# Optimization experiments

Measured on AMD Instinct MI355X. Metric: run time of the kernel, lower is better.

## Reference

```python
import jax, jax.numpy as jnp
import numpy as np

B, C, H, W = 8, 256, 64, 64
K = 64  # tfam_channels

def _conv3x3(x, w, b):
    # x: [B,C,H,W], w: [O,I,3,3]
    y = jax.lax.conv_general_dilated(x, w, window_strides=(1, 1), padding='SAME',
                                     dimension_numbers=('NCHW', 'OIHW', 'NCHW'))
    return y + b[None, :, None, None]

def setup_inputs() -> dict:
    key = jax.random.key(0)
    ks = jax.random.split(key, 5)
    s1 = 1.0 / np.sqrt(C)
    s3 = 1.0 / np.sqrt(C * 9)
    return {
        'x': jax.random.normal(ks[0], (B, C, H, W), jnp.float32),
        'top_w': jax.random.normal(ks[1], (K, C), jnp.float32) * s1,
        'top_b': jnp.zeros((K,), jnp.float32),
        'center_w': jax.random.normal(ks[2], (K, C), jnp.float32) * s1,
        'center_b': jnp.zeros((K,), jnp.float32),
        'bottom_w': jax.random.normal(ks[3], (C, C, 3, 3), jnp.float32) * s3,
        'bottom_b': jnp.zeros((C,), jnp.float32),
        'out_w': jax.random.normal(ks[4], (C, C, 3, 3), jnp.float32) * s3,
        'out_b': jnp.zeros((C,), jnp.float32),
    }

def reference(x, top_w, top_b, center_w, center_b, bottom_w, bottom_b, out_w, out_b):
    b, c, h, w = x.shape
    hw = h * w
    # 1x1 convs as channel contractions
    x_top = jnp.einsum('bchw,kc->bkhw', x, top_w) + top_b[None, :, None, None]
    x_center = jnp.einsum('bchw,kc->bkhw', x, center_w) + center_b[None, :, None, None]
    x_bottom = _conv3x3(x, bottom_w, bottom_b)

    x_top = x_top.reshape(b, -1, hw)                     # [B,K,HW]
    x_center = x_center.reshape(b, -1, hw)               # [B,K,HW]
    x_bot = x_bottom.reshape(b, c, hw).transpose(0, 2, 1)  # [B,HW,C]

    sp_map = jnp.einsum('bkn,bkm->bnm', x_center, x_top)  # [B,HW,HW]
    # global softmax over the entire flattened map per batch element
    sp_map = jax.nn.softmax(sp_map.reshape(b, -1), axis=1).reshape(b, hw, hw)
    sp_map = jnp.einsum('bnm,bmc->bnc', sp_map, x_bot)    # [B,HW,C]
    # faithful raw reshape (as in the torch code: no transpose)
    sp_map = sp_map.reshape(b, c, h, w)
    y = x + sp_map
    return _conv3x3(y, out_w, out_b)
```

## Files before the change

### kernel.cpp

```cpp
#include <hip/hip_runtime.h>

using bf16x8 = __attribute__((ext_vector_type(8))) short;
using f16x8  = __attribute__((ext_vector_type(8))) _Float16;
using f32x4  = __attribute__((ext_vector_type(4))) float;

#define DEVI static __device__ __forceinline__

DEVI unsigned short f2bf(float f){
  unsigned u = __builtin_bit_cast(unsigned, f);
  u += 0x7fffu + ((u >> 16) & 1u);
  return (unsigned short)(u >> 16);
}
DEVI float bf2f(unsigned short h){
  unsigned u = ((unsigned)h) << 16;
  return __builtin_bit_cast(float, u);
}
DEVI unsigned short f2h(float f){
  _Float16 h = (_Float16)f;
  return __builtin_bit_cast(unsigned short, h);
}
DEVI f32x4 zf4(){ f32x4 z; z[0]=0.f; z[1]=0.f; z[2]=0.f; z[3]=0.f; return z; }

__global__ __launch_bounds__(256) void k_prep(
    const float* __restrict__ top_w, const float* __restrict__ cen_w,
    const float* __restrict__ bot_w, const float* __restrict__ out_w,
    float* __restrict__ wTt, float* __restrict__ wTc,
    unsigned short* __restrict__ apb, unsigned short* __restrict__ apo){
  int i = blockIdx.x * 256 + threadIdx.x;
  if (i < 64 * 256){
    int c = i >> 6, k = i & 63;
    wTt[i] = top_w[k * 256 + c];
    wTc[i] = cen_w[k * 256 + c];
  }
  if (i < 9 * 256 * 256){
    int tau = i >> 16, oc = i & 65535;
    apb[i] = f2bf(bot_w[oc * 9 + tau]);
    apo[i] = f2bf(out_w[oc * 9 + tau]);
  }
}

__global__ __launch_bounds__(256) void k_topcenter(
    const float* __restrict__ x,
    const float* __restrict__ wTt, const float* __restrict__ wTc,
    const float* __restrict__ top_b, const float* __restrict__ cen_b,
    unsigned short* __restrict__ tT16, unsigned short* __restrict__ cT16){
  __shared__ float xs[16][256];
  int bid = blockIdx.x;
  int b = bid & 7, z = (bid >> 3) & 1, nt = (bid >> 4) & 15, kq = bid >> 8;
  int t = threadIdx.x;
  int n = nt * 256 + t;
  int k0 = kq * 16;
  const float* wT   = z ? wTc : wTt;
  const float* bias = z ? cen_b : top_b;
  unsigned short* o16 = z ? cT16 : tT16;
  const float scale = z ? 1.0f : 1.4426950408889634f;
  const float* xb = x + ((size_t)b << 20);

  float acc[16];
  #pragma unroll
  for (int k = 0; k < 16; k++) acc[k] = 0.f;

  for (int cc = 0; cc < 256; cc += 16){
    __syncthreads();
    #pragma unroll
    for (int r = 0; r < 16; r++)
      xs[r][t] = xb[((size_t)(cc + r) << 12) + nt * 256 + t];
    __syncthreads();
    #pragma unroll
    for (int r = 0; r < 16; r++){
      float xv = xs[r][t];
      const float* wr = wT + (cc + r) * 64 + k0;
      #pragma unroll
      for (int k = 0; k < 16; k++) acc[k] = fmaf(wr[k], xv, acc[k]);
    }
  }
  size_t base = (((size_t)b << 12) + n) * 64 + k0;
  #pragma unroll
  for (int k8 = 0; k8 < 16; k8 += 8){
    bf16x8 v8;
    #pragma unroll
    for (int j = 0; j < 8; j++)
      v8[j] = (short)f2h((acc[k8 + j] + bias[k0 + k8 + j]) * scale);
    *(bf16x8*)(o16 + base + k8) = v8;
  }
}

__global__ __launch_bounds__(256) void k_transx(
    const float* __restrict__ x, unsigned short* __restrict__ ocl){
  __shared__ float tile[32][33];
  int b = blockIdx.z, ct = blockIdx.y, pt = blockIdx.x;
  int tx = threadIdx.x & 31, ty = threadIdx.x >> 5;
  size_t bo = (size_t)b << 20;
  int c0 = ct * 32, p0 = pt * 32;
  #pragma unroll
  for (int q = 0; q < 4; q++){
    int c = c0 + ty + q * 8;
    tile[ty + q * 8][tx] = x[bo + ((size_t)c << 12) + p0 + tx];
  }
  __syncthreads();
  #pragma unroll
  for (int q = 0; q < 4; q++){
    int p = p0 + ty + q * 8;
    ocl[bo + ((size_t)p << 8) + c0 + tx] = f2bf(tile[tx][ty + q * 8]);
  }
}

__global__ __launch_bounds__(256) void k_transy(
    const float* __restrict__ x, const unsigned short* __restrict__ U0,
    const unsigned short* __restrict__ U1, const float* __restrict__ Z,
    unsigned short* __restrict__ ocl){
  __shared__ float tile[32][33];
  int b = blockIdx.z, ct = blockIdx.y, pt = blockIdx.x;
  int tx = threadIdx.x & 31, ty = threadIdx.x >> 5;
  size_t bo = (size_t)b << 20;
  int c0 = ct * 32, p0 = pt * 32;
  float invZ = 1.0f / Z[b];
  #pragma unroll
  for (int q = 0; q < 4; q++){
    int c = c0 + ty + q * 8;
    size_t idx = bo + ((size_t)c << 12) + p0 + tx;
    float u = bf2f(U0[idx]);
    if (U1) u += bf2f(U1[idx]);
    tile[ty + q * 8][tx] = fmaf(u, invZ, x[idx]);
  }
  __syncthreads();
  #pragma unroll
  for (int q = 0; q < 4; q++){
    int p = p0 + ty + q * 8;
    ocl[bo + ((size_t)p << 8) + c0 + tx] = f2bf(tile[tx][ty + q * 8]);
  }
}

template<int OUTF32>
__global__ __launch_bounds__(256, 4) void k_conv3(
    const unsigned short* __restrict__ incl,
    const unsigned short* __restrict__ ap,
    const float* __restrict__ bias, void* __restrict__ outp){
  __shared__ unsigned short Xs[3][64][72];
  int bid = blockIdx.x;
  int b = bid & 7, h = (bid >> 3) & 63, oh = bid >> 9;
  int t = threadIdx.x, wv = t >> 6, l = t & 63, lr = l & 15, g = l >> 4;
  int o0 = oh * 128 + wv * 32;
  const unsigned short* inb = incl + ((size_t)b << 20);

  f32x4 acc[2][4];
  #pragma unroll
  for (int a = 0; a < 2; a++)
    #pragma unroll
    for (int c = 0; c < 4; c++) acc[a][c] = zf4();

  int sw = t >> 2, sco = (t & 3) * 16;
  const bf16x8 zero8 = {0,0,0,0,0,0,0,0};

  bf16x8 st[3][2];
  #pragma unroll
  for (int r = 0; r < 3; r++){
    int h2 = h + r - 1;
    bool v = (unsigned)h2 < 64u;
    #pragma unroll
    for (int u = 0; u < 2; u++)
      st[r][u] = v ? *(const bf16x8*)(inb + (((size_t)(h2 * 64 + sw)) << 8)
                                      + sco + u * 8)
                   : zero8;
  }

  for (int cc = 0; cc < 256; cc += 64){
    __syncthreads();
    #pragma unroll
    for (int r = 0; r < 3; r++)
      #pragma unroll
      for (int u = 0; u < 2; u++)
        *(bf16x8*)(&Xs[r][sw][sco + u * 8]) = st[r][u];
    __syncthreads();
    if (cc < 192){
      #pragma unroll
      for (int r = 0; r < 3; r++){
        int h2 = h + r - 1;
        bool v = (unsigned)h2 < 64u;
        #pragma unroll
        for (int u = 0; u < 2; u++)
          st[r][u] = v ? *(const bf16x8*)(inb + (((size_t)(h2 * 64 + sw)) << 8)
                                          + cc + 64 + sco + u * 8)
                       : zero8;
      }
    }
    #pragma unroll
    for (int tau = 0; tau < 9; tau++){
      int dy = tau / 3 - 1, dx = tau % 3 - 1;
      #pragma unroll
      for (int kf = 0; kf < 2; kf++){
        bf16x8 af[2];
        #pragma unroll
        for (int of = 0; of < 2; of++)
          af[of] = *(const bf16x8*)(ap + ((size_t)tau << 16)
                     + ((o0 + of * 16 + lr) << 8) + cc + kf * 32 + 8 * g);
        bf16x8 bv[4];
        #pragma unroll
        for (int pf = 0; pf < 4; pf++){
          int wsrc = pf * 16 + lr + dx;
          bv[pf] = ((unsigned)wsrc < 64u)
                 ? *(const bf16x8*)(&Xs[dy + 1][wsrc][kf * 32 + 8 * g])
                 : zero8;
        }
        #pragma unroll
        for (int of = 0; of < 2; of++)
          #pragma unroll
          for (int pf = 0; pf < 4; pf++)
            acc[of][pf] = __builtin_amdgcn_mfma_f32_16x16x32_bf16(af[of], bv[pf], acc[of][pf], 0, 0, 0);
      }
    }
  }
  #pragma unroll
  for (int of = 0; of < 2; of++){
    int ob = o0 + of * 16 + 4 * g;
    #pragma unroll
    for (int pf = 0; pf < 4; pf++){
      int p = h * 64 + pf * 16 + lr;
      #pragma unroll
      for (int i = 0; i < 4; i++){
        int o = ob + i;
        float v = acc[of][pf][i] + bias[o];
        size_t oi = ((size_t)b << 20) + ((size_t)o << 12) + p;
        if (OUTF32) ((float*)outp)[oi] = v;
        else        ((unsigned short*)outp)[oi] = f2bf(v);
      }
    }
  }
}

__global__ __launch_bounds__(256, 4) void k_pv(
    const unsigned short* __restrict__ tT16, const unsigned short* __restrict__ cT16,
    const unsigned short* __restrict__ xbot,
    unsigned short* __restrict__ U0, unsigned short* __restrict__ U1,
    float* __restrict__ rsum, int nsteps){
  __shared__ unsigned short Pl[2][64 * 32];
  __shared__ unsigned short Xl[2][256 * 32];
  int bid = blockIdx.x;
  int b = bid & 7, nt = (bid >> 3) & 63, mh = bid >> 9;
  int t = threadIdx.x, wv = t >> 6, l = t & 63, lr = l & 15, g = l >> 4;
  int n0 = nt * 64;
  const unsigned short* xbb = xbot + ((size_t)b << 20);
  unsigned short* Ub = mh ? U1 : U0;

  f16x8 ch[2][2];
  #pragma unroll
  for (int kf = 0; kf < 2; kf++)
    #pragma unroll
    for (int nf = 0; nf < 2; nf++)
      ch[kf][nf] = *(const f16x8*)(cT16
          + (((size_t)b << 12) + n0 + (wv >> 1) * 32 + nf * 16 + lr) * 64
          + kf * 32 + 8 * g);

  f32x4 acc[4][4];
  #pragma unroll
  for (int a = 0; a < 4; a++)
    #pragma unroll
    for (int c = 0; c < 4; c++) acc[a][c] = zf4();
  float racc = 0.f;
  unsigned pk[2][2];

  const unsigned short* tb = tT16
      + (((size_t)b << 12) + (size_t)mh * 2048 + (wv & 1) * 16 + lr) * 64 + 8 * g;

  int rl = l >> 2;
  int swzl = (rl & 3) ^ (rl >> 2);
  const unsigned short* gstage = xbb
      + ((size_t)(wv * 64 + rl) << 12) + (size_t)mh * 2048
      + (((l & 3) ^ swzl) << 3);

  auto gll = [&](int buf, int step){
    const unsigned short* gs = gstage + (size_t)step * 32;
    #pragma unroll
    for (int j = 0; j < 4; j++)
      __builtin_amdgcn_global_load_lds(
          (const __attribute__((address_space(1))) void*)(gs + ((size_t)(16 * j) << 12)),
          (__attribute__((address_space(3))) void*)(&Xl[buf][(wv * 64 + j * 16) * 32]),
          16, 0, 0);
  };

  auto sphase = [&](f16x8 A0, f16x8 A1){
    f32x4 sa[2];
    sa[0] = zf4(); sa[1] = zf4();
    #pragma unroll
    for (int nf = 0; nf < 2; nf++)
      sa[nf] = __builtin_amdgcn_mfma_f32_16x16x32_f16(A0, ch[0][nf], sa[nf], 0, 0, 0);
    #pragma unroll
    for (int nf = 0; nf < 2; nf++)
      sa[nf] = __builtin_amdgcn_mfma_f32_16x16x32_f16(A1, ch[1][nf], sa[nf], 0, 0, 0);
    #pragma unroll
    for (int nf = 0; nf < 2; nf++){
      float e0 = __builtin_amdgcn_exp2f(sa[nf][0]);
      float e1 = __builtin_amdgcn_exp2f(sa[nf][1]);
      float e2 = __builtin_amdgcn_exp2f(sa[nf][2]);
      float e3 = __builtin_amdgcn_exp2f(sa[nf][3]);
      racc += (e0 + e1) + (e2 + e3);
      pk[nf][0] = (unsigned)f2bf(e0) | ((unsigned)f2bf(e1) << 16);
      pk[nf][1] = (unsigned)f2bf(e2) | ((unsigned)f2bf(e3) << 16);
    }
  };

  int mt2 = (wv & 1) * 2 + (g >> 1);
  auto plwrite = [&](int buf){
    #pragma unroll
    for (int nf = 0; nf < 2; nf++){
      int n = (wv >> 1) * 32 + nf * 16 + lr;
      int slot = mt2 ^ (lr & 3) ^ (lr >> 2);
      unsigned* pp = (unsigned*)(&Pl[buf][n * 32 + slot * 8 + (g & 1) * 4]);
      pp[0] = pk[nf][0];
      pp[1] = pk[nf][1];
    }
  };

  int rswz = (g ^ (lr & 3) ^ (lr >> 2)) * 8;
  auto pv = [&](int buf){
    bf16x8 pa[4];
    #pragma unroll
    for (int nf = 0; nf < 4; nf++)
      pa[nf] = *(const bf16x8*)(&Pl[buf][(nf * 16 + lr) * 32 + rswz]);
    #pragma unroll
    for (int cf = 0; cf < 4; cf++){
      bf16x8 bx = *(const bf16x8*)(&Xl[buf][(wv * 64 + cf * 16 + lr) * 32 + rswz]);
      #pragma unroll
      for (int nf = 0; nf < 4; nf++)
        acc[nf][cf] = __builtin_amdgcn_mfma_f32_16x16x32_bf16(pa[nf], bx, acc[nf][cf], 0, 0, 0);
    }
  };

  f16x8 a0 = *(const f16x8*)(tb);
  f16x8 a1 = *(const f16x8*)(tb + 32);
  gll(0, 0);
  sphase(a0, a1);
  a0 = *(const f16x8*)(tb + 2048);
  a1 = *(const f16x8*)(tb + 2048 + 32);
  plwrite(0);
  __syncthreads();

  for (int ms = 0; ms < nsteps; ms++){
    int cur = ms & 1, nxt = cur ^ 1;
    if (ms + 1 < nsteps){
      gll(nxt, ms + 1);
      sphase(a0, a1);
      if (ms + 2 < nsteps){
        a0 = *(const f16x8*)(tb + (size_t)(ms + 2) * 2048);
        a1 = *(const f16x8*)(tb + (size_t)(ms + 2) * 2048 + 32);
      }
    }
    pv(cur);
    if (ms + 1 < nsteps) plwrite(nxt);
    __syncthreads();
  }

  #pragma unroll
  for (int nf = 0; nf < 4; nf++)
    #pragma unroll
    for (int cf = 0; cf < 4; cf++)
      #pragma unroll
      for (int i = 0; i < 4; i++){
        int n = n0 + nf * 16 + 4 * g + i;
        int c = wv * 64 + cf * 16 + lr;
        __builtin_nontemporal_store(f2bf(acc[nf][cf][i]),
            &Ub[((size_t)b << 20) + ((size_t)n << 8) + c]);
      }
  racc += __shfl_xor(racc, 1);
  racc += __shfl_xor(racc, 2);
  racc += __shfl_xor(racc, 4);
  racc += __shfl_xor(racc, 8);
  racc += __shfl_xor(racc, 16);
  racc += __shfl_xor(racc, 32);
  if (l == 0) rsum[(size_t)bid * 4 + wv] = racc;
}

__global__ __launch_bounds__(256) void k_rsum(const float* __restrict__ r,
                                              float* __restrict__ Z, int msplit){
  __shared__ float red[256];
  int b = blockIdx.x, t = threadIdx.x;
  int total = 256 * msplit;
  float s = 0.f;
  for (int s2 = t; s2 < total; s2 += 256)
    s += r[(size_t)(b + 8 * (s2 >> 2)) * 4 + (s2 & 3)];
  red[t] = s;
  __syncthreads();
  for (int o = 128; o > 0; o >>= 1){
    if (t < o) red[t] += red[t + o];
    __syncthreads();
  }
  if (t == 0) Z[b] = red[0];
}

extern "C" void kernel_launch(void* const* d_in, const int* in_sizes, int n_in,
                              void* d_out, int out_size, void* d_ws, size_t ws_size,
                              hipStream_t stream) {
  const float* x     = (const float*)d_in[0];
  const float* top_w = (const float*)d_in[1];
  const float* top_b = (const float*)d_in[2];
  const float* cen_w = (const float*)d_in[3];
  const float* cen_b = (const float*)d_in[4];
  const float* bot_w = (const float*)d_in[5];
  const float* bot_b = (const float*)d_in[6];
  const float* out_w = (const float*)d_in[7];
  const float* out_b = (const float*)d_in[8];
  float* out = (float*)d_out;

  constexpr size_t MB = 1ull << 20;
  int msplit = (ws_size >= 80 * MB) ? 2 : 1;

  char* p = (char*)d_ws;
  unsigned short* U0 = (unsigned short*)p;     p += 16 * MB;
  unsigned short* U1 = nullptr;
  if (msplit == 2){ U1 = (unsigned short*)p;   p += 16 * MB; }
  unsigned short* tT16 = (unsigned short*)p;   p += 4 * MB;
  unsigned short* cT16 = (unsigned short*)p;   p += 4 * MB;
  unsigned short* xbot = (unsigned short*)p;   p += 16 * MB;
  unsigned short* xcl  = (unsigned short*)p;   p += 16 * MB;
  float* wTt = (float*)p;                      p += 65536;
  float* wTc = (float*)p;                      p += 65536;
  unsigned short* apb = (unsigned short*)p;    p += 1179648;
  unsigned short* apo = (unsigned short*)p;    p += 1179648;
  float* r = (float*)p;                        p += 65536;
  float* Z = (float*)p;

  k_prep<<<2304, 256, 0, stream>>>(top_w, cen_w, bot_w, out_w, wTt, wTc, apb, apo);
  k_topcenter<<<dim3(1024), 256, 0, stream>>>(x, wTt, wTc, top_b, cen_b,
                                              tT16, cT16);
  k_transx<<<dim3(128, 8, 8), 256, 0, stream>>>(x, xcl);
  k_conv3<0><<<dim3(1024), 256, 0, stream>>>(xcl, apb, bot_b, (void*)xbot);
  k_pv<<<dim3(512 * msplit), 256, 0, stream>>>(tT16, cT16, xbot, U0,
                                               msplit == 2 ? U1 : U0, r,
                                               2048 / (32 * msplit) * 2);
  k_rsum<<<8, 256, 0, stream>>>(r, Z, msplit);
  k_transy<<<dim3(128, 8, 8), 256, 0, stream>>>(x, U0, U1, Z, xcl);
  k_conv3<1><<<dim3(1024), 256, 0, stream>>>(xcl, apo, out_b, (void*)out);
}
```

Before: 333.5 us.

## Double k_pv query tile to 128 rows and restructure LDS layout without swizzle

The attention-like PV kernel now processes 128 query positions per block instead of 64. Each staged X tile is therefore reused by twice as many MFMA operations, halving the global reads of x_bot per output. The LDS tiles for X and P move to a slot-major [k-slot][row][8] layout and drop the XOR swizzle, and the rsum reduction takes its slot count from the host. Accumulator registers double and launch bounds drop to 2 blocks per SIMD, which lowers occupancy and halves the grid, and the unswizzled layout may cause LDS bank conflicts.

```diff
diff --git a/kernel.cpp b/kernel.cpp
--- a/kernel.cpp
+++ b/kernel.cpp
@@ -228,67 +228,64 @@
   }
 }
 
-__global__ __launch_bounds__(256, 4) void k_pv(
+__global__ __launch_bounds__(256, 2) void k_pv(
     const unsigned short* __restrict__ tT16, const unsigned short* __restrict__ cT16,
     const unsigned short* __restrict__ xbot,
     unsigned short* __restrict__ U0, unsigned short* __restrict__ U1,
     float* __restrict__ rsum, int nsteps){
-  __shared__ unsigned short Pl[2][64 * 32];
-  __shared__ unsigned short Xl[2][256 * 32];
+  __shared__ unsigned short Xl[2][4][256][8];
+  __shared__ unsigned short Pl[2][4][128][8];
   int bid = blockIdx.x;
-  int b = bid & 7, nt = (bid >> 3) & 63, mh = bid >> 9;
+  int b = bid & 7, nt = (bid >> 3) & 31, mh = bid >> 8;
   int t = threadIdx.x, wv = t >> 6, l = t & 63, lr = l & 15, g = l >> 4;
-  int n0 = nt * 64;
+  int n0 = nt * 128;
   const unsigned short* xbb = xbot + ((size_t)b << 20);
   unsigned short* Ub = mh ? U1 : U0;
 
-  f16x8 ch[2][2];
+  f16x8 ch[2][4];
   #pragma unroll
   for (int kf = 0; kf < 2; kf++)
     #pragma unroll
-    for (int nf = 0; nf < 2; nf++)
+    for (int nf = 0; nf < 4; nf++)
       ch[kf][nf] = *(const f16x8*)(cT16
-          + (((size_t)b << 12) + n0 + (wv >> 1) * 32 + nf * 16 + lr) * 64
+          + (((size_t)b << 12) + n0 + (wv >> 1) * 64 + nf * 16 + lr) * 64
           + kf * 32 + 8 * g);
 
-  f32x4 acc[4][4];
-  #pragma unroll
-  for (int a = 0; a < 4; a++)
+  f32x4 acc[8][4];
+  #pragma unroll
+  for (int a = 0; a < 8; a++)
     #pragma unroll
     for (int c = 0; c < 4; c++) acc[a][c] = zf4();
   float racc = 0.f;
-  unsigned pk[2][2];
+  unsigned pk[4][2];
 
   const unsigned short* tb = tT16
       + (((size_t)b << 12) + (size_t)mh * 2048 + (wv & 1) * 16 + lr) * 64 + 8 * g;
 
-  int rl = l >> 2;
-  int swzl = (rl & 3) ^ (rl >> 2);
-  const unsigned short* gstage = xbb
-      + ((size_t)(wv * 64 + rl) << 12) + (size_t)mh * 2048
-      + (((l & 3) ^ swzl) << 3);
+  const unsigned short* gsrc = xbb + ((size_t)(wv * 64 + l) << 12)
+                             + (size_t)mh * 2048;
 
   auto gll = [&](int buf, int step){
-    const unsigned short* gs = gstage + (size_t)step * 32;
     #pragma unroll
     for (int j = 0; j < 4; j++)
       __builtin_amdgcn_global_load_lds(
-          (const __attribute__((address_space(1))) void*)(gs + ((size_t)(16 * j) << 12)),
-          (__attribute__((address_space(3))) void*)(&Xl[buf][(wv * 64 + j * 16) * 32]),
+          (const __attribute__((address_space(1))) void*)(gsrc + step * 32 + j * 8),
+          (__attribute__((address_space(3))) void*)(&Xl[buf][j][wv * 64][0]),
           16, 0, 0);
   };
 
   auto sphase = [&](f16x8 A0, f16x8 A1){
-    f32x4 sa[2];
-    sa[0] = zf4(); sa[1] = zf4();
-    #pragma unroll
-    for (int nf = 0; nf < 2; nf++)
+    f32x4 sa[4];
+    #pragma unroll
+    for (int nf = 0; nf < 4; nf++) sa[nf] = zf4();
+    #pragma unroll
+    for (int nf = 0; nf < 4; nf++)
       sa[nf] = __builtin_amdgcn_mfma_f32_16x16x32_f16(A0, ch[0][nf], sa[nf], 0, 0, 0);
     #pragma unroll
-    for (int nf = 0; nf < 2; nf++)
+    for (int nf = 0; nf < 4; nf++)
       sa[nf] = __builtin_amdgcn_mfma_f32_16x16x32_f16(A1, ch[1][nf], sa[nf], 0, 0, 0);
     #pragma unroll
-    for (int nf = 0; nf < 2; nf++){
+    for (int nf = 0; nf < 4; nf++){
       float e0 = __builtin_amdgcn_exp2f(sa[nf][0]);
       float e1 = __builtin_amdgcn_exp2f(sa[nf][1]);
       float e2 = __builtin_amdgcn_exp2f(sa[nf][2]);
@@ -302,26 +299,24 @@
   int mt2 = (wv & 1) * 2 + (g >> 1);
   auto plwrite = [&](int buf){
     #pragma unroll
-    for (int nf = 0; nf < 2; nf++){
-      int n = (wv >> 1) * 32 + nf * 16 + lr;
-      int slot = mt2 ^ (lr & 3) ^ (lr >> 2);
-      unsigned* pp = (unsigned*)(&Pl[buf][n * 32 + slot * 8 + (g & 1) * 4]);
+    for (int nf = 0; nf < 4; nf++){
+      int n = (wv >> 1) * 64 + nf * 16 + lr;
+      unsigned* pp = (unsigned*)(&Pl[buf][mt2][n][(g & 1) * 4]);
       pp[0] = pk[nf][0];
       pp[1] = pk[nf][1];
     }
   };
 
-  int rswz = (g ^ (lr & 3) ^ (lr >> 2)) * 8;
   auto pv = [&](int buf){
-    bf16x8 pa[4];
-    #pragma unroll
-    for (int nf = 0; nf < 4; nf++)
-      pa[nf] = *(const bf16x8*)(&Pl[buf][(nf * 16 + lr) * 32 + rswz]);
+    bf16x8 pa[8];
+    #pragma unroll
+    for (int nf = 0; nf < 8; nf++)
+      pa[nf] = *(const bf16x8*)(&Pl[buf][g][nf * 16 + lr][0]);
     #pragma unroll
     for (int cf = 0; cf < 4; cf++){
-      bf16x8 bx = *(const bf16x8*)(&Xl[buf][(wv * 64 + cf * 16 + lr) * 32 + rswz]);
-      #pragma unroll
-      for (int nf = 0; nf < 4; nf++)
+      bf16x8 bx = *(const bf16x8*)(&Xl[buf][g][wv * 64 + cf * 16 + lr][0]);
+      #pragma unroll
+      for (int nf = 0; nf < 8; nf++)
         acc[nf][cf] = __builtin_amdgcn_mfma_f32_16x16x32_bf16(pa[nf], bx, acc[nf][cf], 0, 0, 0);
     }
   };
@@ -351,7 +346,7 @@
   }
 
   #pragma unroll
-  for (int nf = 0; nf < 4; nf++)
+  for (int nf = 0; nf < 8; nf++)
     #pragma unroll
     for (int cf = 0; cf < 4; cf++)
       #pragma unroll
@@ -371,10 +366,9 @@
 }
 
 __global__ __launch_bounds__(256) void k_rsum(const float* __restrict__ r,
-                                              float* __restrict__ Z, int msplit){
+                                              float* __restrict__ Z, int total){
   __shared__ float red[256];
   int b = blockIdx.x, t = threadIdx.x;
-  int total = 256 * msplit;
   float s = 0.f;
   for (int s2 = t; s2 < total; s2 += 256)
     s += r[(size_t)(b + 8 * (s2 >> 2)) * 4 + (s2 & 3)];
@@ -419,15 +413,18 @@
   float* r = (float*)p;                        p += 65536;
   float* Z = (float*)p;
 
+  int grid_pv = 8 * 32 * msplit;
+  int nsteps  = (4096 / msplit) / 32;
+  int slots   = (grid_pv / 8) * 4;
+
   k_prep<<<2304, 256, 0, stream>>>(top_w, cen_w, bot_w, out_w, wTt, wTc, apb, apo);
   k_topcenter<<<dim3(1024), 256, 0, stream>>>(x, wTt, wTc, top_b, cen_b,
                                               tT16, cT16);
   k_transx<<<dim3(128, 8, 8), 256, 0, stream>>>(x, xcl);
   k_conv3<0><<<dim3(1024), 256, 0, stream>>>(xcl, apb, bot_b, (void*)xbot);
-  k_pv<<<dim3(512 * msplit), 256, 0, stream>>>(tT16, cT16, xbot, U0,
-                                               msplit == 2 ? U1 : U0, r,
-                                               2048 / (32 * msplit) * 2);
-  k_rsum<<<8, 256, 0, stream>>>(r, Z, msplit);
+  k_pv<<<dim3(grid_pv), 256, 0, stream>>>(tT16, cT16, xbot, U0,
+                                          msplit == 2 ? U1 : U0, r, nsteps);
+  k_rsum<<<8, 256, 0, stream>>>(r, Z, slots);
   k_transy<<<dim3(128, 8, 8), 256, 0, stream>>>(x, U0, U1, Z, xcl);
   k_conv3<1><<<dim3(1024), 256, 0, stream>>>(xcl, apo, out_b, (void*)out);
 }
```

Result: no change. 336.9 us (+1.0%).

## Restructure PV loop: k-major LDS layout, hardware bf16 pack, deferred exp

Applied to the files above, without the earlier changes.

The attention PV kernel's shared-memory tiles move from a swizzled row-major layout to a k-chunk-major layout ([buf][kchunk][row][8]). Each lane's global_load_lds now pulls contiguous 16-byte chunks of its own row, and fragment reads need no XOR swizzle. The exp/pack/LDS-write of the next score tile is moved after the current step's PV MFMAs, so the score MFMA latency is hidden behind matrix work. Software float-to-bf16 rounding is replaced with the v_cvt_pk_bf16_f32 instruction. The unswizzled layout may bring back LDS bank conflicts, and the k_rsum argument is now a slot count.

```diff
diff --git a/kernel.cpp b/kernel.cpp
--- a/kernel.cpp
+++ b/kernel.cpp
@@ -20,6 +20,11 @@
   return __builtin_bit_cast(unsigned short, h);
 }
 DEVI f32x4 zf4(){ f32x4 z; z[0]=0.f; z[1]=0.f; z[2]=0.f; z[3]=0.f; return z; }
+DEVI unsigned cvtpk(float lo, float hi){
+  unsigned r;
+  asm("v_cvt_pk_bf16_f32 %0, %1, %2" : "=v"(r) : "v"(lo), "v"(hi));
+  return r;
+}
 
 __global__ __launch_bounds__(256) void k_prep(
     const float* __restrict__ top_w, const float* __restrict__ cen_w,
@@ -233,8 +238,8 @@
     const unsigned short* __restrict__ xbot,
     unsigned short* __restrict__ U0, unsigned short* __restrict__ U1,
     float* __restrict__ rsum, int nsteps){
-  __shared__ unsigned short Pl[2][64 * 32];
-  __shared__ unsigned short Xl[2][256 * 32];
+  __shared__ unsigned short Xl[2][4][256][8];
+  __shared__ unsigned short Pl[2][4][64][8];
   int bid = blockIdx.x;
   int b = bid & 7, nt = (bid >> 3) & 63, mh = bid >> 9;
   int t = threadIdx.x, wv = t >> 6, l = t & 63, lr = l & 15, g = l >> 4;
@@ -257,36 +262,34 @@
     #pragma unroll
     for (int c = 0; c < 4; c++) acc[a][c] = zf4();
   float racc = 0.f;
-  unsigned pk[2][2];
 
   const unsigned short* tb = tT16
       + (((size_t)b << 12) + (size_t)mh * 2048 + (wv & 1) * 16 + lr) * 64 + 8 * g;
 
-  int rl = l >> 2;
-  int swzl = (rl & 3) ^ (rl >> 2);
-  const unsigned short* gstage = xbb
-      + ((size_t)(wv * 64 + rl) << 12) + (size_t)mh * 2048
-      + (((l & 3) ^ swzl) << 3);
-
-  auto gll = [&](int buf, int step){
-    const unsigned short* gs = gstage + (size_t)step * 32;
+  const unsigned short* gsrc = xbb + ((size_t)(wv * 64 + l) << 12)
+                             + (size_t)mh * 2048;
+
+  f16x8 a0 = *(const f16x8*)(tb);
+  f16x8 a1 = *(const f16x8*)(tb + 32);
+  int mt2 = (wv & 1) * 2 + (g >> 1);
+
+  {
     #pragma unroll
     for (int j = 0; j < 4; j++)
       __builtin_amdgcn_global_load_lds(
-          (const __attribute__((address_space(1))) void*)(gs + ((size_t)(16 * j) << 12)),
-          (__attribute__((address_space(3))) void*)(&Xl[buf][(wv * 64 + j * 16) * 32]),
+          (const __attribute__((address_space(1))) void*)(gsrc + j * 8),
+          (__attribute__((address_space(3))) void*)(&Xl[0][j][wv * 64][0]),
           16, 0, 0);
-  };
-
-  auto sphase = [&](f16x8 A0, f16x8 A1){
     f32x4 sa[2];
     sa[0] = zf4(); sa[1] = zf4();
     #pragma unroll
     for (int nf = 0; nf < 2; nf++)
-      sa[nf] = __builtin_amdgcn_mfma_f32_16x16x32_f16(A0, ch[0][nf], sa[nf], 0, 0, 0);
+      sa[nf] = __builtin_amdgcn_mfma_f32_16x16x32_f16(a0, ch[0][nf], sa[nf], 0, 0, 0);
     #pragma unroll
     for (int nf = 0; nf < 2; nf++)
-      sa[nf] = __builtin_amdgcn_mfma_f32_16x16x32_f16(A1, ch[1][nf], sa[nf], 0, 0, 0);
+      sa[nf] = __builtin_amdgcn_mfma_f32_16x16x32_f16(a1, ch[1][nf], sa[nf], 0, 0, 0);
+    a0 = *(const f16x8*)(tb + 2048);
+    a1 = *(const f16x8*)(tb + 2048 + 32);
     #pragma unroll
     for (int nf = 0; nf < 2; nf++){
       float e0 = __builtin_amdgcn_exp2f(sa[nf][0]);
@@ -294,59 +297,64 @@
       float e2 = __builtin_amdgcn_exp2f(sa[nf][2]);
       float e3 = __builtin_amdgcn_exp2f(sa[nf][3]);
       racc += (e0 + e1) + (e2 + e3);
-      pk[nf][0] = (unsigned)f2bf(e0) | ((unsigned)f2bf(e1) << 16);
-      pk[nf][1] = (unsigned)f2bf(e2) | ((unsigned)f2bf(e3) << 16);
-    }
-  };
-
-  int mt2 = (wv & 1) * 2 + (g >> 1);
-  auto plwrite = [&](int buf){
-    #pragma unroll
-    for (int nf = 0; nf < 2; nf++){
       int n = (wv >> 1) * 32 + nf * 16 + lr;
-      int slot = mt2 ^ (lr & 3) ^ (lr >> 2);
-      unsigned* pp = (unsigned*)(&Pl[buf][n * 32 + slot * 8 + (g & 1) * 4]);
-      pp[0] = pk[nf][0];
-      pp[1] = pk[nf][1];
-    }
-  };
-
-  int rswz = (g ^ (lr & 3) ^ (lr >> 2)) * 8;
-  auto pv = [&](int buf){
-    bf16x8 pa[4];
-    #pragma unroll
-    for (int nf = 0; nf < 4; nf++)
-      pa[nf] = *(const bf16x8*)(&Pl[buf][(nf * 16 + lr) * 32 + rswz]);
-    #pragma unroll
-    for (int cf = 0; cf < 4; cf++){
-      bf16x8 bx = *(const bf16x8*)(&Xl[buf][(wv * 64 + cf * 16 + lr) * 32 + rswz]);
-      #pragma unroll
-      for (int nf = 0; nf < 4; nf++)
-        acc[nf][cf] = __builtin_amdgcn_mfma_f32_16x16x32_bf16(pa[nf], bx, acc[nf][cf], 0, 0, 0);
-    }
-  };
-
-  f16x8 a0 = *(const f16x8*)(tb);
-  f16x8 a1 = *(const f16x8*)(tb + 32);
-  gll(0, 0);
-  sphase(a0, a1);
-  a0 = *(const f16x8*)(tb + 2048);
-  a1 = *(const f16x8*)(tb + 2048 + 32);
-  plwrite(0);
-  __syncthreads();
+      unsigned* pp = (unsigned*)(&Pl[0][mt2][n][(g & 1) * 4]);
+      pp[0] = cvtpk(e0, e1);
+      pp[1] = cvtpk(e2, e3);
+    }
+    __syncthreads();
+  }
 
   for (int ms = 0; ms < nsteps; ms++){
     int cur = ms & 1, nxt = cur ^ 1;
-    if (ms + 1 < nsteps){
-      gll(nxt, ms + 1);
-      sphase(a0, a1);
+    bool more = (ms + 1 < nsteps);
+    f32x4 sa[2];
+    sa[0] = zf4(); sa[1] = zf4();
+    if (more){
+      #pragma unroll
+      for (int j = 0; j < 4; j++)
+        __builtin_amdgcn_global_load_lds(
+            (const __attribute__((address_space(1))) void*)(gsrc + (ms + 1) * 32 + j * 8),
+            (__attribute__((address_space(3))) void*)(&Xl[nxt][j][wv * 64][0]),
+            16, 0, 0);
+      #pragma unroll
+      for (int nf = 0; nf < 2; nf++)
+        sa[nf] = __builtin_amdgcn_mfma_f32_16x16x32_f16(a0, ch[0][nf], sa[nf], 0, 0, 0);
+      #pragma unroll
+      for (int nf = 0; nf < 2; nf++)
+        sa[nf] = __builtin_amdgcn_mfma_f32_16x16x32_f16(a1, ch[1][nf], sa[nf], 0, 0, 0);
       if (ms + 2 < nsteps){
         a0 = *(const f16x8*)(tb + (size_t)(ms + 2) * 2048);
         a1 = *(const f16x8*)(tb + (size_t)(ms + 2) * 2048 + 32);
       }
     }
-    pv(cur);
-    if (ms + 1 < nsteps) plwrite(nxt);
+    {
+      bf16x8 pa[4];
+      #pragma unroll
+      for (int nf = 0; nf < 4; nf++)
+        pa[nf] = *(const bf16x8*)(&Pl[cur][g][nf * 16 + lr][0]);
+      #pragma unroll
+      for (int cf = 0; cf < 4; cf++){
+        bf16x8 bx = *(const bf16x8*)(&Xl[cur][g][wv * 64 + cf * 16 + lr][0]);
+        #pragma unroll
+        for (int nf = 0; nf < 4; nf++)
+          acc[nf][cf] = __builtin_amdgcn_mfma_f32_16x16x32_bf16(pa[nf], bx, acc[nf][cf], 0, 0, 0);
+      }
+    }
+    if (more){
+      #pragma unroll
+      for (int nf = 0; nf < 2; nf++){
+        float e0 = __builtin_amdgcn_exp2f(sa[nf][0]);
+        float e1 = __builtin_amdgcn_exp2f(sa[nf][1]);
+        float e2 = __builtin_amdgcn_exp2f(sa[nf][2]);
+        float e3 = __builtin_amdgcn_exp2f(sa[nf][3]);
+        racc += (e0 + e1) + (e2 + e3);
+        int n = (wv >> 1) * 32 + nf * 16 + lr;
+        unsigned* pp = (unsigned*)(&Pl[nxt][mt2][n][(g & 1) * 4]);
+        pp[0] = cvtpk(e0, e1);
+        pp[1] = cvtpk(e2, e3);
+      }
+    }
     __syncthreads();
   }
 
@@ -371,10 +379,9 @@
 }
 
 __global__ __launch_bounds__(256) void k_rsum(const float* __restrict__ r,
-                                              float* __restrict__ Z, int msplit){
+                                              float* __restrict__ Z, int total){
   __shared__ float red[256];
   int b = blockIdx.x, t = threadIdx.x;
-  int total = 256 * msplit;
   float s = 0.f;
   for (int s2 = t; s2 < total; s2 += 256)
     s += r[(size_t)(b + 8 * (s2 >> 2)) * 4 + (s2 & 3)];
@@ -419,15 +426,18 @@
   float* r = (float*)p;                        p += 65536;
   float* Z = (float*)p;
 
+  int grid_pv = 8 * 64 * msplit;
+  int nsteps  = (4096 / msplit) / 32;
+  int slots   = (grid_pv / 8) * 4;
+
   k_prep<<<2304, 256, 0, stream>>>(top_w, cen_w, bot_w, out_w, wTt, wTc, apb, apo);
   k_topcenter<<<dim3(1024), 256, 0, stream>>>(x, wTt, wTc, top_b, cen_b,
                                               tT16, cT16);
   k_transx<<<dim3(128, 8, 8), 256, 0, stream>>>(x, xcl);
   k_conv3<0><<<dim3(1024), 256, 0, stream>>>(xcl, apb, bot_b, (void*)xbot);
-  k_pv<<<dim3(512 * msplit), 256, 0, stream>>>(tT16, cT16, xbot, U0,
-                                               msplit == 2 ? U1 : U0, r,
-                                               2048 / (32 * msplit) * 2);
-  k_rsum<<<8, 256, 0, stream>>>(r, Z, msplit);
+  k_pv<<<dim3(grid_pv), 256, 0, stream>>>(tT16, cT16, xbot, U0,
+                                          msplit == 2 ? U1 : U0, r, nsteps);
+  k_rsum<<<8, 256, 0, stream>>>(r, Z, slots);
   k_transy<<<dim3(128, 8, 8), 256, 0, stream>>>(x, U0, U1, Z, xcl);
   k_conv3<1><<<dim3(1024), 256, 0, stream>>>(xcl, apo, out_b, (void*)out);
 }
```

Result: slower. 429.9 us (+28.9%).
